# Performance work log

Measured on AMD Instinct MI355X. Metric: run time of the kernel, lower is better.

The kernel has to match this reference:

```python
import jax, jax.numpy as jnp
import numpy as np

N_NODES = 100000
N_EDGES = 3200000
F_IN = 128
HID = 16


def gcn_conv(x, W, b, src, dst, n_nodes):
    # PyG GCNConv: h = x @ W; add self-loops; deg on dst; sym-normalized scatter-add; + bias
    h = x @ W  # [N, out]
    loop = jnp.arange(n_nodes, dtype=src.dtype)
    s = jnp.concatenate([src, loop])
    d = jnp.concatenate([dst, loop])
    ones = jnp.ones(s.shape[0], dtype=h.dtype)
    deg = jax.ops.segment_sum(ones, d, num_segments=n_nodes)  # in-degree incl self-loop
    dinv = jnp.where(deg > 0, jax.lax.rsqrt(deg), 0.0)
    norm = dinv[s] * dinv[d]  # [E+N]
    msg = h[s] * norm[:, None]
    out = jax.ops.segment_sum(msg, d, num_segments=n_nodes)
    return out + b


def setup_inputs() -> dict:
    key = jax.random.key(0)
    ks = jax.random.split(key, 8)
    x = jax.random.normal(ks[0], (N_NODES, F_IN), dtype=jnp.float32)
    edge_index = jax.random.randint(ks[1], (2, N_EDGES), 0, N_NODES, dtype=jnp.int32)
    sc1 = 1.0 / np.sqrt(F_IN)
    sc2 = 1.0 / np.sqrt(HID)
    sc3 = 1.0 / np.sqrt(2 * HID)
    W1 = jax.random.uniform(ks[2], (F_IN, HID), jnp.float32, -sc1, sc1)
    b1 = jnp.zeros((HID,), jnp.float32)
    W2 = jax.random.uniform(ks[3], (HID, HID), jnp.float32, -sc2, sc2)
    b2 = jnp.zeros((HID,), jnp.float32)
    Wf = jax.random.uniform(ks[4], (2 * HID, 1), jnp.float32, -sc3, sc3)
    bf = jax.random.uniform(ks[5], (1,), jnp.float32, -sc3, sc3)
    return {"x": x, "edge_index": edge_index, "W1": W1, "b1": b1, "W2": W2, "b2": b2, "Wf": Wf, "bf": bf}


def reference(x, edge_index, W1, b1, W2, b2, Wf, bf):
    src, dst = edge_index[0], edge_index[1]
    h = gcn_conv(x, W1, b1, src, dst, N_NODES)
    h = jax.nn.relu(h)  # dropout is identity in eval mode
    h = gcn_conv(h, W2, b2, src, dst, N_NODES)
    edge_emb = jnp.concatenate([h[src], h[dst]], axis=1)  # [E, 2*HID]
    pred = edge_emb @ Wf + bf  # [E, 1]
    return pred.squeeze(-1)
```

## Files before the change

kernel.cpp:

```cpp
#include <hip/hip_runtime.h>
#include <hip/hip_fp16.h>

#define N_NODES 100000
#define N_EDGES 3200000
#define F_IN 128
#define HID 16

#define SHIFT 8
#define NPB 256
#define NB 391
#define CHUNK 4096
#define NCHUNK ((N_EDGES + CHUNK - 1) / CHUNK)
#define MAXBE 9216
#define HALFR 4608
#define SMAX 9
#define CPAD 16

__device__ __forceinline__ float2 h2f(unsigned u) {
    __half2 h;
    *reinterpret_cast<unsigned*>(&h) = u;
    return __half22float2(h);
}
__device__ __forceinline__ unsigned f2h(float a, float b) {
    __half2 h = __floats2half2_rn(a, b);
    return *reinterpret_cast<unsigned*>(&h);
}

__global__ __launch_bounds__(512) void k_part(const int* __restrict__ src,
                                              const int* __restrict__ dst,
                                              int* __restrict__ cursor,
                                              unsigned* __restrict__ ebuf, int E) {
    __shared__ int lcnt[512];
    __shared__ int lcur[512];
    __shared__ int dlt[512];
    __shared__ int wsum[8], wpre[8];
    __shared__ unsigned sbuf[CHUNK];
    __shared__ unsigned short sbkt[CHUNK];
    int t = threadIdx.x;
    int lane = t & 63, wid = t >> 6;
    lcnt[t] = 0;
    __syncthreads();
    int e0 = blockIdx.x * CHUNK;
    int ne = min(CHUNK, E - e0);
    for (int e = t; e < ne; e += 512) atomicAdd(&lcnt[dst[e0 + e] >> SHIFT], 1);
    __syncthreads();
    int v = lcnt[t];
    int s = v;
#pragma unroll
    for (int o = 1; o < 64; o <<= 1) {
        int u = __shfl_up(s, o);
        if (lane >= o) s += u;
    }
    if (lane == 63) wsum[wid] = s;
    __syncthreads();
    if (t == 0) {
        int r = 0;
#pragma unroll
        for (int k = 0; k < 8; k++) {
            wpre[k] = r;
            r += wsum[k];
        }
    }
    __syncthreads();
    int o = s + wpre[wid] - v;
    lcur[t] = o;
    if (t < NB && v) dlt[t] = t * MAXBE + atomicAdd(&cursor[t * CPAD], v) - o;
    __syncthreads();
    for (int e = t; e < ne; e += 512) {
        int d = dst[e0 + e];
        int b = d >> SHIFT;
        int p = atomicAdd(&lcur[b], 1);
        sbuf[p] = ((unsigned)src[e0 + e] << SHIFT) | (unsigned)(d & (NPB - 1));
        sbkt[p] = (unsigned short)b;
    }
    __syncthreads();
    for (int k = t; k < ne; k += 512) ebuf[k + dlt[sbkt[k]]] = sbuf[k];
}

__global__ __launch_bounds__(512) void k_sort2h(const unsigned* __restrict__ ebuf,
                                                const int* __restrict__ cursor,
                                                int* __restrict__ ebuf2,
                                                int2* __restrict__ offseA,
                                                int2* __restrict__ offseB, int N) {
    __shared__ int hist[NPB];
    __shared__ int cur[NPB];
    __shared__ int wsum[4], wpre[4];
    __shared__ int sbufS[HALFR];
    int t = threadIdx.x;
    int lane = t & 63, wid = t >> 6;
    int b = blockIdx.x >> 1, h = blockIdx.x & 1;
    if (t < NPB) hist[t] = 0;
    __syncthreads();
    int cnt = min(cursor[b * CPAD], MAXBE);
    int mid = cnt >> 1;
    int lo = h ? mid : 0;
    int ne = (h ? cnt : mid) - lo;
    int base_r = b * MAXBE + lo;
    unsigned eu[SMAX];
    int nq = 0;
    for (int e = t; e < ne; e += 512) eu[nq++] = ebuf[base_r + e];
    for (int q = 0; q < nq; q++) atomicAdd(&hist[eu[q] & (NPB - 1u)], 1);
    __syncthreads();
    int base_w = blockIdx.x * HALFR;
    int v = (t < NPB) ? hist[t] : 0;
    if (t < NPB) {
        int s = v;
#pragma unroll
        for (int o = 1; o < 64; o <<= 1) {
            int u = __shfl_up(s, o);
            if (lane >= o) s += u;
        }
        if (lane == 63) wsum[wid] = s;
        hist[t] = s;
    }
    __syncthreads();
    if (t == 0) {
        int r = 0;
#pragma unroll
        for (int k = 0; k < 4; k++) {
            wpre[k] = r;
            r += wsum[k];
        }
    }
    __syncthreads();
    if (t < NPB) {
        int ex = hist[t] + wpre[wid] - v;
        cur[t] = ex;
        int i = b * NPB + t;
        if (i < N) {
            int2 oe = make_int2(base_w + ex, base_w + ex + v);
            if (h == 0) offseA[i] = oe;
            else        offseB[i] = oe;
        }
    }
    __syncthreads();
    for (int q = 0; q < nq; q++) {
        int p = atomicAdd(&cur[eu[q] & (NPB - 1u)], 1);
        sbufS[p] = (int)(eu[q] >> SHIFT);
    }
    __syncthreads();
    for (int k = t; k < ne; k += 512) ebuf2[base_w + k] = sbufS[k];
}

__global__ __launch_bounds__(256) void k_gemm1(const float* __restrict__ x,
                                               const float* __restrict__ W1,
                                               const int2* __restrict__ offseA,
                                               const int2* __restrict__ offseB,
                                               float* __restrict__ dinv,
                                               uint4* __restrict__ gt, int N) {
    __shared__ float w1s[F_IN * HID];
    for (int idx = threadIdx.x; idx < F_IN * HID; idx += 256) w1s[idx] = W1[idx];
    __syncthreads();
    int t = threadIdx.x;
    int r = t >> 1, hf = t & 1;
    int i = blockIdx.x * 128 + r;
    float acc[HID];
#pragma unroll
    for (int n = 0; n < HID; n++) acc[n] = 0.f;
    if (i < N) {
        const float4* xr = (const float4*)(x + (size_t)i * F_IN + hf * (F_IN / 2));
#pragma unroll 4
        for (int k4 = 0; k4 < F_IN / 8; k4++) {
            float4 xv = xr[k4];
            int k = hf * (F_IN / 2) + k4 * 4;
#pragma unroll
            for (int n = 0; n < HID; n++) {
                acc[n] += xv.x * w1s[(k + 0) * HID + n] + xv.y * w1s[(k + 1) * HID + n] +
                          xv.z * w1s[(k + 2) * HID + n] + xv.w * w1s[(k + 3) * HID + n];
            }
        }
    }
#pragma unroll
    for (int n = 0; n < HID; n++) acc[n] += __shfl_xor(acc[n], 1);
    if (hf == 0 && i < N) {
        int2 oA = offseA[i], oB = offseB[i];
        int deg = (oA.y - oA.x) + (oB.y - oB.x);
        float dv = rsqrtf((float)(deg + 1));
        dinv[i] = dv;
        uint4 w0, w1;
        w0.x = f2h(acc[0] * dv, acc[1] * dv);
        w0.y = f2h(acc[2] * dv, acc[3] * dv);
        w0.z = f2h(acc[4] * dv, acc[5] * dv);
        w0.w = f2h(acc[6] * dv, acc[7] * dv);
        w1.x = f2h(acc[8] * dv, acc[9] * dv);
        w1.y = f2h(acc[10] * dv, acc[11] * dv);
        w1.z = f2h(acc[12] * dv, acc[13] * dv);
        w1.w = f2h(acc[14] * dv, acc[15] * dv);
        gt[2 * (size_t)i] = w0;
        gt[2 * (size_t)i + 1] = w1;
    }
}

__global__ __launch_bounds__(256) void k_gather1(const unsigned* __restrict__ gtu,
                                                 const int2* __restrict__ offseA,
                                                 const int2* __restrict__ offseB,
                                                 const int* __restrict__ ebuf2,
                                                 const float* __restrict__ dinv,
                                                 const float* __restrict__ b1,
                                                 unsigned* __restrict__ htu, int N) {
    int i = (blockIdx.x * 256 + threadIdx.x) >> 6;
    int lane = threadIdx.x & 63;
    if (i >= N) return;
    int eo = lane >> 3, s = lane & 7;
    int2 oA = offseA[i], oB = offseB[i];
    float2 a = make_float2(0.f, 0.f);
    for (int e = oA.x + eo; e < oA.y; e += 8) {
        float2 f = h2f(gtu[ebuf2[e] * 8 + s]);
        a.x += f.x;
        a.y += f.y;
    }
    for (int e = oB.x + eo; e < oB.y; e += 8) {
        float2 f = h2f(gtu[ebuf2[e] * 8 + s]);
        a.x += f.x;
        a.y += f.y;
    }
    a.x += __shfl_xor(a.x, 8);  a.y += __shfl_xor(a.y, 8);
    a.x += __shfl_xor(a.x, 16); a.y += __shfl_xor(a.y, 16);
    a.x += __shfl_xor(a.x, 32); a.y += __shfl_xor(a.y, 32);
    if (eo == 0) {
        float2 f = h2f(gtu[i * 8 + s]);
        a.x += f.x;
        a.y += f.y;
        float dv = dinv[i];
        float2 bb = ((const float2*)b1)[s];
        float o0 = fmaxf(dv * a.x + bb.x, 0.f);
        float o1 = fmaxf(dv * a.y + bb.y, 0.f);
        htu[i * 8 + s] = f2h(o0, o1);
    }
}

__global__ __launch_bounds__(256) void k_gemm2q(const uint4* __restrict__ ht,
                                                const float* __restrict__ W2,
                                                const float* __restrict__ dinv,
                                                const float* __restrict__ Wf,
                                                float2* __restrict__ q, int N) {
    __shared__ float w[HID * HID];
    __shared__ float wfs[32];
    w[threadIdx.x] = W2[threadIdx.x];
    if (threadIdx.x < 32) wfs[threadIdx.x] = Wf[threadIdx.x];
    __syncthreads();
    int i = blockIdx.x * 256 + threadIdx.x;
    if (i >= N) return;
    uint4 r0 = ht[2 * (size_t)i], r1 = ht[2 * (size_t)i + 1];
    float hv[HID];
    float2 f;
    f = h2f(r0.x); hv[0] = f.x; hv[1] = f.y;
    f = h2f(r0.y); hv[2] = f.x; hv[3] = f.y;
    f = h2f(r0.z); hv[4] = f.x; hv[5] = f.y;
    f = h2f(r0.w); hv[6] = f.x; hv[7] = f.y;
    f = h2f(r1.x); hv[8] = f.x; hv[9] = f.y;
    f = h2f(r1.y); hv[10] = f.x; hv[11] = f.y;
    f = h2f(r1.z); hv[12] = f.x; hv[13] = f.y;
    f = h2f(r1.w); hv[14] = f.x; hv[15] = f.y;
    float out[HID];
#pragma unroll
    for (int n = 0; n < HID; n++) out[n] = 0.f;
#pragma unroll
    for (int k = 0; k < HID; k++) {
#pragma unroll
        for (int n = 0; n < HID; n++) out[n] += hv[k] * w[k * HID + n];
    }
    float qs = 0.f, qd = 0.f;
#pragma unroll
    for (int n = 0; n < HID; n++) {
        qs += out[n] * wfs[n];
        qd += out[n] * wfs[16 + n];
    }
    float dv = dinv[i];
    q[i] = make_float2(qs * dv, qd * dv);
}

__global__ __launch_bounds__(256) void k_gather2(const float2* __restrict__ q,
                                                 const int2* __restrict__ offseA,
                                                 const int2* __restrict__ offseB,
                                                 const int* __restrict__ ebuf2,
                                                 const float* __restrict__ dinv,
                                                 const float* __restrict__ b2,
                                                 const float* __restrict__ Wf,
                                                 const float* __restrict__ bf,
                                                 float2* __restrict__ nd, int N) {
    __shared__ float2 C;
    if (threadIdx.x == 0) {
        float c1 = 0.f, c2 = 0.f;
#pragma unroll
        for (int k = 0; k < HID; k++) {
            c1 += b2[k] * Wf[k];
            c2 += b2[k] * Wf[16 + k];
        }
        C = make_float2(c1, c2 + bf[0]);
    }
    __syncthreads();
    int grp = threadIdx.x >> 4, l = threadIdx.x & 15;
    int i = blockIdx.x * 16 + grp;
    if (i >= N) return;
    int2 oA = offseA[i], oB = offseB[i];
    float2 a = make_float2(0.f, 0.f);
    for (int e = oA.x + l; e < oA.y; e += 16) {
        float2 qq = q[ebuf2[e]];
        a.x += qq.x;
        a.y += qq.y;
    }
    for (int e = oB.x + l; e < oB.y; e += 16) {
        float2 qq = q[ebuf2[e]];
        a.x += qq.x;
        a.y += qq.y;
    }
    a.x += __shfl_xor(a.x, 1); a.y += __shfl_xor(a.y, 1);
    a.x += __shfl_xor(a.x, 2); a.y += __shfl_xor(a.y, 2);
    a.x += __shfl_xor(a.x, 4); a.y += __shfl_xor(a.y, 4);
    a.x += __shfl_xor(a.x, 8); a.y += __shfl_xor(a.y, 8);
    if (l == 0) {
        float2 self = q[i];
        float dv = dinv[i];
        nd[i] = make_float2(dv * (a.x + self.x) + C.x, dv * (a.y + self.y) + C.y);
    }
}

__global__ __launch_bounds__(256) void k_edge2(const int* __restrict__ src,
                                               const int* __restrict__ dst,
                                               const float2* __restrict__ nd,
                                               float* __restrict__ pred, int E) {
    int e = blockIdx.x * 256 + threadIdx.x;
    if (e >= E) return;
    pred[e] = nd[src[e]].x + nd[dst[e]].y;
}

extern "C" void kernel_launch(void* const* d_in, const int* in_sizes, int n_in,
                              void* d_out, int out_size, void* d_ws, size_t ws_size,
                              hipStream_t stream) {
    const float* x  = (const float*)d_in[0];
    const int*   ei = (const int*)d_in[1];
    const float* W1 = (const float*)d_in[2];
    const float* b1 = (const float*)d_in[3];
    const float* W2 = (const float*)d_in[4];
    const float* b2 = (const float*)d_in[5];
    const float* Wf = (const float*)d_in[6];
    const float* bf = (const float*)d_in[7];
    float* pred = (float*)d_out;

    const int N = N_NODES, E = N_EDGES;
    const int* src = ei;
    const int* dst = ei + E;

    char* w = (char*)d_ws;
    int*      cursor = (int*)(w + 0x0);
    float*    dinv   = (float*)(w + 0x10000);
    int2*     offseA = (int2*)(w + 0x80000);
    int2*     offseB = (int2*)(w + 0x150000);
    float2*   nd     = (float2*)(w + 0x220000);
    unsigned* ebuf   = (unsigned*)(w + 0x3C0000);
    uint4*    gt     = (uint4*)(w + 0x3C0000);
    float2*   q      = (float2*)(w + 0x700000);
    int*      ebuf2  = (int*)(w + 0x11A0000);
    uint4*    ht     = (uint4*)(w + 0x1F70000);

    const int B = 256;
    int gE   = (E + B - 1) / B;
    int gN   = (N + B - 1) / B;
    int gN2  = (N + 127) / 128;
    int gN64 = (N * 64) / B;
    int gN16 = (N + 15) / 16;

    hipMemsetAsync(cursor, 0, NB * CPAD * sizeof(int), stream);
    k_part<<<NCHUNK, 512, 0, stream>>>(src, dst, cursor, ebuf, E);
    k_sort2h<<<2 * NB, 512, 0, stream>>>(ebuf, cursor, ebuf2, offseA, offseB, N);
    k_gemm1<<<gN2, B, 0, stream>>>(x, W1, offseA, offseB, dinv, gt, N);
    k_gather1<<<gN64, B, 0, stream>>>((const unsigned*)gt, offseA, offseB, ebuf2, dinv, b1,
                                      (unsigned*)ht, N);
    k_gemm2q<<<gN, B, 0, stream>>>(ht, W2, dinv, Wf, q, N);
    k_gather2<<<gN16, B, 0, stream>>>(q, offseA, offseB, ebuf2, dinv, b2, Wf, bf, nd, N);
    k_edge2<<<gE, B, 0, stream>>>(src, dst, nd, pred, E);
}
```

Measured before the change: 186.0 us.

## Fuse second-layer projection into gather1 via folded W2·Wf vector

Removes the separate k_gemm2q kernel. The W2 @ Wf product is folded into a 32-float vector in shared memory, so the relu'd aggregated features are turned straight into the per-node source and destination scalars q using a shuffle reduction. This drops the fp16 ht intermediate write and its reread, plus one launch. Each block now handles four nodes and first stages their contiguous edge-index ranges into shared memory. That adds a __syncthreads, and it relies on the GCAP=768 shared buffer never overflowing for high-degree node groups.

```diff
diff --git a/kernel.cpp b/kernel.cpp
--- a/kernel.cpp
+++ b/kernel.cpp
@@ -15,6 +15,7 @@
 #define HALFR 4608
 #define SMAX 9
 #define CPAD 16
+#define GCAP 768
 
 __device__ __forceinline__ float2 h2f(unsigned u) {
     __half2 h;
@@ -197,20 +198,41 @@
                                                  const int* __restrict__ ebuf2,
                                                  const float* __restrict__ dinv,
                                                  const float* __restrict__ b1,
-                                                 unsigned* __restrict__ htu, int N) {
-    int i = (blockIdx.x * 256 + threadIdx.x) >> 6;
-    int lane = threadIdx.x & 63;
-    if (i >= N) return;
+                                                 const float* __restrict__ W2,
+                                                 const float* __restrict__ Wf,
+                                                 float2* __restrict__ q, int N) {
+    __shared__ int eAs[GCAP];
+    __shared__ int eBs[GCAP];
+    __shared__ float v2[32];
+    int t = threadIdx.x;
+    if (t < 32) {
+        int k = t & 15, hi = t >> 4;
+        float s = 0.f;
+#pragma unroll
+        for (int n = 0; n < HID; n++) s += W2[k * HID + n] * Wf[hi * HID + n];
+        v2[t] = s;
+    }
+    int i0 = blockIdx.x * 4;
+    int sA = offseA[i0].x, tA = offseA[i0 + 3].y;
+    int sB = offseB[i0].x, tB = offseB[i0 + 3].y;
+    int lA = tA - sA, lB = tB - sB;
+    for (int k = t; k < lA; k += 256) eAs[k] = ebuf2[sA + k];
+    for (int k = t; k < lB; k += 256) eBs[k] = ebuf2[sB + k];
+    __syncthreads();
+    int wid = t >> 6, lane = t & 63;
+    int i = i0 + wid;
     int eo = lane >> 3, s = lane & 7;
     int2 oA = offseA[i], oB = offseB[i];
+    int a0 = oA.x - sA, a1 = oA.y - sA;
+    int c0 = oB.x - sB, c1 = oB.y - sB;
     float2 a = make_float2(0.f, 0.f);
-    for (int e = oA.x + eo; e < oA.y; e += 8) {
-        float2 f = h2f(gtu[ebuf2[e] * 8 + s]);
+    for (int e = a0 + eo; e < a1; e += 8) {
+        float2 f = h2f(gtu[eAs[e] * 8 + s]);
         a.x += f.x;
         a.y += f.y;
     }
-    for (int e = oB.x + eo; e < oB.y; e += 8) {
-        float2 f = h2f(gtu[ebuf2[e] * 8 + s]);
+    for (int e = c0 + eo; e < c1; e += 8) {
+        float2 f = h2f(gtu[eBs[e] * 8 + s]);
         a.x += f.x;
         a.y += f.y;
     }
@@ -225,49 +247,13 @@
         float2 bb = ((const float2*)b1)[s];
         float o0 = fmaxf(dv * a.x + bb.x, 0.f);
         float o1 = fmaxf(dv * a.y + bb.y, 0.f);
-        htu[i * 8 + s] = f2h(o0, o1);
-    }
-}
-
-__global__ __launch_bounds__(256) void k_gemm2q(const uint4* __restrict__ ht,
-                                                const float* __restrict__ W2,
-                                                const float* __restrict__ dinv,
-                                                const float* __restrict__ Wf,
-                                                float2* __restrict__ q, int N) {
-    __shared__ float w[HID * HID];
-    __shared__ float wfs[32];
-    w[threadIdx.x] = W2[threadIdx.x];
-    if (threadIdx.x < 32) wfs[threadIdx.x] = Wf[threadIdx.x];
-    __syncthreads();
-    int i = blockIdx.x * 256 + threadIdx.x;
-    if (i >= N) return;
-    uint4 r0 = ht[2 * (size_t)i], r1 = ht[2 * (size_t)i + 1];
-    float hv[HID];
-    float2 f;
-    f = h2f(r0.x); hv[0] = f.x; hv[1] = f.y;
-    f = h2f(r0.y); hv[2] = f.x; hv[3] = f.y;
-    f = h2f(r0.z); hv[4] = f.x; hv[5] = f.y;
-    f = h2f(r0.w); hv[6] = f.x; hv[7] = f.y;
-    f = h2f(r1.x); hv[8] = f.x; hv[9] = f.y;
-    f = h2f(r1.y); hv[10] = f.x; hv[11] = f.y;
-    f = h2f(r1.z); hv[12] = f.x; hv[13] = f.y;
-    f = h2f(r1.w); hv[14] = f.x; hv[15] = f.y;
-    float out[HID];
-#pragma unroll
-    for (int n = 0; n < HID; n++) out[n] = 0.f;
-#pragma unroll
-    for (int k = 0; k < HID; k++) {
-#pragma unroll
-        for (int n = 0; n < HID; n++) out[n] += hv[k] * w[k * HID + n];
-    }
-    float qs = 0.f, qd = 0.f;
-#pragma unroll
-    for (int n = 0; n < HID; n++) {
-        qs += out[n] * wfs[n];
-        qd += out[n] * wfs[16 + n];
-    }
-    float dv = dinv[i];
-    q[i] = make_float2(qs * dv, qd * dv);
+        float qs = o0 * v2[2 * s] + o1 * v2[2 * s + 1];
+        float qd = o0 * v2[16 + 2 * s] + o1 * v2[16 + 2 * s + 1];
+        qs += __shfl_xor(qs, 1); qd += __shfl_xor(qd, 1);
+        qs += __shfl_xor(qs, 2); qd += __shfl_xor(qd, 2);
+        qs += __shfl_xor(qs, 4); qd += __shfl_xor(qd, 4);
+        if (s == 0) q[i] = make_float2(dv * qs, dv * qd);
+    }
 }
 
 __global__ __launch_bounds__(256) void k_gather2(const float2* __restrict__ q,
@@ -352,22 +338,19 @@
     uint4*    gt     = (uint4*)(w + 0x3C0000);
     float2*   q      = (float2*)(w + 0x700000);
     int*      ebuf2  = (int*)(w + 0x11A0000);
-    uint4*    ht     = (uint4*)(w + 0x1F70000);
 
     const int B = 256;
     int gE   = (E + B - 1) / B;
-    int gN   = (N + B - 1) / B;
     int gN2  = (N + 127) / 128;
-    int gN64 = (N * 64) / B;
+    int gN4  = N / 4;
     int gN16 = (N + 15) / 16;
 
     hipMemsetAsync(cursor, 0, NB * CPAD * sizeof(int), stream);
     k_part<<<NCHUNK, 512, 0, stream>>>(src, dst, cursor, ebuf, E);
     k_sort2h<<<2 * NB, 512, 0, stream>>>(ebuf, cursor, ebuf2, offseA, offseB, N);
     k_gemm1<<<gN2, B, 0, stream>>>(x, W1, offseA, offseB, dinv, gt, N);
-    k_gather1<<<gN64, B, 0, stream>>>((const unsigned*)gt, offseA, offseB, ebuf2, dinv, b1,
-                                      (unsigned*)ht, N);
-    k_gemm2q<<<gN, B, 0, stream>>>(ht, W2, dinv, Wf, q, N);
+    k_gather1<<<gN4, B, 0, stream>>>((const unsigned*)gt, offseA, offseB, ebuf2, dinv, b1,
+                                     W2, Wf, q, N);
     k_gather2<<<gN16, B, 0, stream>>>(q, offseA, offseB, ebuf2, dinv, b2, Wf, bf, nd, N);
     k_edge2<<<gE, B, 0, stream>>>(src, dst, nd, pred, E);
 }
```

New measurement: 181.7 us. 2.3% less time.
